# Performance work log

Hardware: AMD Instinct MI355X
Metric: run time of the kernel (lower is better)

Reference implementation:

```python
import jax, jax.numpy as jnp
import numpy as np

N = 50000      # nodes
E = 800000     # edges (before self-loops)
IN = 512       # in_dim
HID = 128      # hidden_dim
HEADS = 4
NEG_SLOPE = 0.2


def setup_inputs() -> dict:
    key = jax.random.key(0)
    ks = jax.random.split(key, 20)
    s = 0.05
    inp = {
        'x': jax.random.normal(ks[0], (N, IN), jnp.float32),
        'edge_index': jax.random.randint(ks[1], (2, E), 0, N, dtype=jnp.int32),
        # layer 0: GATConv(IN -> HID, heads=HEADS)
        'W0': jax.random.normal(ks[2], (HEADS * HID, IN), jnp.float32) * s,
        'a_src0': jax.random.normal(ks[3], (HEADS, HID), jnp.float32) * s,
        'a_dst0': jax.random.normal(ks[4], (HEADS, HID), jnp.float32) * s,
        'b0': jnp.zeros((HEADS * HID,), jnp.float32),
        # layer 1: GATConv(HEADS*HID -> HID, heads=HEADS)
        'W1': jax.random.normal(ks[5], (HEADS * HID, HEADS * HID), jnp.float32) * s,
        'a_src1': jax.random.normal(ks[6], (HEADS, HID), jnp.float32) * s,
        'a_dst1': jax.random.normal(ks[7], (HEADS, HID), jnp.float32) * s,
        'b1': jnp.zeros((HEADS * HID,), jnp.float32),
        # layer 2: GATConv(HEADS*HID -> HID, heads=1)
        'W2': jax.random.normal(ks[8], (HID, HEADS * HID), jnp.float32) * s,
        'a_src2': jax.random.normal(ks[9], (1, HID), jnp.float32) * s,
        'a_dst2': jax.random.normal(ks[10], (1, HID), jnp.float32) * s,
        'b2': jnp.zeros((HID,), jnp.float32),
        # output heads
        'Wv': jax.random.normal(ks[11], (HID, HID), jnp.float32) * s,
        'bv': jnp.zeros((HID,), jnp.float32),
        'Wt': jax.random.normal(ks[12], (HID, HID), jnp.float32) * s,
        'bt': jnp.zeros((HID,), jnp.float32),
    }
    return inp


def _gat_conv(x, src, dst, W, a_src, a_dst, bias, heads, n_nodes):
    """PyG-style GATConv (eval mode, att_dropout=0, self-loops pre-added)."""
    ch = a_src.shape[-1]
    h = (x @ W.T).reshape(n_nodes, heads, ch)            # [N,H,C]
    alpha_s = jnp.einsum('nhc,hc->nh', h, a_src)          # [N,H]
    alpha_d = jnp.einsum('nhc,hc->nh', h, a_dst)          # [N,H]
    e = alpha_s[src] + alpha_d[dst]                       # [E,H]
    e = jnp.where(e > 0, e, NEG_SLOPE * e)                # leaky_relu(0.2)
    # segment softmax over destination nodes
    m = jax.ops.segment_max(e, dst, num_segments=n_nodes)  # [N,H]
    e = jnp.exp(e - m[dst])
    z = jax.ops.segment_sum(e, dst, num_segments=n_nodes)  # [N,H]
    alpha = e / (z[dst] + 1e-16)                          # [E,H]
    msg = h[src] * alpha[:, :, None]                      # [E,H,C]
    out = jax.ops.segment_sum(msg, dst, num_segments=n_nodes)  # [N,H,C]
    return out.reshape(n_nodes, heads * ch) + bias


def reference(x, edge_index, W0, a_src0, a_dst0, b0, W1, a_src1, a_dst1, b1,
              W2, a_src2, a_dst2, b2, Wv, bv, Wt, bt):
    n = x.shape[0]
    loops = jnp.arange(n, dtype=edge_index.dtype)
    src = jnp.concatenate([edge_index[0], loops])
    dst = jnp.concatenate([edge_index[1], loops])

    h = _gat_conv(x, src, dst, W0, a_src0, a_dst0, b0, HEADS, n)
    h = jax.nn.relu(h)                                    # dropout is no-op in eval
    h = _gat_conv(h, src, dst, W1, a_src1, a_dst1, b1, HEADS, n)
    h = jax.nn.relu(h)
    h = _gat_conv(h, src, dst, W2, a_src2, a_dst2, b2, 1, n)  # [N,HID]

    x_vision = jax.nn.relu(h @ Wv.T + bv)
    x_text = jax.nn.relu(h @ Wt.T + bt)
    return (h, x_vision, x_text)
```

## Files before the change

### kernel.cpp

```cpp
#include <hip/hip_runtime.h>
#include <hip/hip_bf16.h>
#include <math.h>

typedef __bf16 bf16;
typedef __bf16 bf16x2 __attribute__((ext_vector_type(2)));
typedef __bf16 bf16x8 __attribute__((ext_vector_type(8)));
typedef float f32x4 __attribute__((ext_vector_type(4)));

#define NNODES 50000
#define NEDGES 800000

static __device__ __forceinline__ void gld_lds16(const void* g, void* l) {
    __builtin_amdgcn_global_load_lds((__attribute__((address_space(1))) void*)g,
                                     (__attribute__((address_space(3))) void*)l,
                                     16, 0, 0);
}

__global__ void detect_kernel(const unsigned int* __restrict__ xw, int* __restrict__ flag)
{
    const int l = threadIdx.x;
    int c = 0;
    for (int i = l; i < 4096; i += 64) {
        const unsigned int b1 = (xw[i] >> 8) & 0x7Fu;
        c += (b1 >= 0x34u && b1 <= 0x43u) ? 1 : 0;
    }
#pragma unroll
    for (int off = 32; off; off >>= 1) c += __shfl_xor(c, off);
    if (l == 0) *flag = (c < 2048) ? 1 : 0;
}

__global__ __launch_bounds__(256) void zero_out_kernel(void* out, long n, const int* __restrict__ flag)
{
    const int fp32 = *flag;
    const long i = (long)blockIdx.x * 256 + threadIdx.x;
    if (i < n) {
        if (fp32) ((float*)out)[i] = 0.f;
        else ((bf16*)out)[i] = (bf16)0.f;
    }
}

__global__ __launch_bounds__(256) void convert_kernel(
    const void* __restrict__ in, bf16* __restrict__ out, int n, const int* __restrict__ flag)
{
    const int fp32 = *flag;
    const int i = blockIdx.x * 256 + threadIdx.x;
    if (i >= n) return;
    out[i] = fp32 ? (bf16)(((const float*)in)[i]) : ((const bf16*)in)[i];
}

struct CvtBatch { const void* in[16]; bf16* out[16]; int n[16]; };

__global__ __launch_bounds__(256) void convert_batch_kernel(CvtBatch b, const int* __restrict__ flag)
{
    const int fp32 = *flag;
    const int it = blockIdx.y;
    const int n = b.n[it];
    const void* in = b.in[it];
    bf16* out = b.out[it];
    for (int i = blockIdx.x * 256 + threadIdx.x; i < n; i += gridDim.x * 256)
        out[i] = fp32 ? (bf16)(((const float*)in)[i]) : ((const bf16*)in)[i];
}

__global__ __launch_bounds__(256) void gemm_bt(
    const bf16* __restrict__ A, const bf16* __restrict__ B,
    bf16* __restrict__ C, int M, int N, int K)
{
    __shared__ __align__(16) bf16 As[128 * 32];
    __shared__ __align__(16) bf16 Bs[128 * 32];
    const int tid  = threadIdx.x;
    const int lane = tid & 63;
    const int w    = tid >> 6;
    const int wm   = (w >> 1) * 64, wn = (w & 1) * 64;
    const int mBase = blockIdx.y * 128, nBase = blockIdx.x * 128;

    f32x4 acc[4][4];
#pragma unroll
    for (int i = 0; i < 4; i++)
#pragma unroll
        for (int j = 0; j < 4; j++)
#pragma unroll
            for (int r = 0; r < 4; r++) acc[i][j][r] = 0.f;

    const int rA   = tid >> 2;
    const int kseg = (tid & 3) * 8;
    int ra0 = mBase + rA;       if (ra0 > M - 1) ra0 = M - 1;
    int ra1 = mBase + rA + 64;  if (ra1 > M - 1) ra1 = M - 1;
    const bf16* gA0 = A + (long)ra0 * K + kseg;
    const bf16* gA1 = A + (long)ra1 * K + kseg;
    const bf16* gB0 = B + (long)(nBase + rA) * K + kseg;
    const bf16* gB1 = B + (long)(nBase + rA + 64) * K + kseg;
    bf16* lA0 = &As[tid * 8];
    bf16* lA1 = &As[(tid + 256) * 8];
    bf16* lB0 = &Bs[tid * 8];
    bf16* lB1 = &Bs[(tid + 256) * 8];

    const int quad = lane >> 4, l16 = lane & 15;

    for (int k0 = 0; k0 < K; k0 += 32) {
        gld_lds16(gA0 + k0, lA0);
        gld_lds16(gA1 + k0, lA1);
        gld_lds16(gB0 + k0, lB0);
        gld_lds16(gB1 + k0, lB1);
        __syncthreads();
        bf16x8 af[4], bfr[4];
#pragma unroll
        for (int i = 0; i < 4; i++) {
            af[i]  = *(const bf16x8*)&As[(wm + i * 16 + l16) * 32 + quad * 8];
            bfr[i] = *(const bf16x8*)&Bs[(wn + i * 16 + l16) * 32 + quad * 8];
        }
#pragma unroll
        for (int i = 0; i < 4; i++)
#pragma unroll
            for (int j = 0; j < 4; j++)
                acc[i][j] = __builtin_amdgcn_mfma_f32_16x16x32_bf16(af[i], bfr[j], acc[i][j], 0, 0, 0);
        __syncthreads();
    }

#pragma unroll
    for (int i = 0; i < 4; i++) {
        const int row0 = mBase + wm + i * 16 + quad * 4;
#pragma unroll
        for (int j = 0; j < 4; j++) {
            const int colg = nBase + wn + j * 16 + l16;
#pragma unroll
            for (int r = 0; r < 4; r++) {
                const int row = row0 + r;
                if (row < M) C[(long)row * N + colg] = (bf16)acc[i][j][r];
            }
        }
    }
}

template <int H>
__global__ __launch_bounds__(H * 64) void alpha_kernel(
    const bf16* __restrict__ h, const bf16* __restrict__ av,
    const bf16* __restrict__ dv, float* __restrict__ as_out,
    float* __restrict__ ad_out)
{
    const int C = 128, HC = H * C;
    const int n = blockIdx.x;
    const int t = threadIdx.x;
    const int ht = t >> 6, l = t & 63;
    const bf16x2 hv = *(const bf16x2*)(h  + (long)n * HC + ht * C + 2 * l);
    const bf16x2 a2 = *(const bf16x2*)(av + ht * C + 2 * l);
    const bf16x2 d2 = *(const bf16x2*)(dv + ht * C + 2 * l);
    const float h0 = (float)hv[0], h1 = (float)hv[1];
    float ps = h0 * (float)a2[0] + h1 * (float)a2[1];
    float pd = h0 * (float)d2[0] + h1 * (float)d2[1];
#pragma unroll
    for (int off = 32; off; off >>= 1) {
        ps += __shfl_xor(ps, off);
        pd += __shfl_xor(pd, off);
    }
    if (l == 0) {
        as_out[(long)n * H + ht] = ps;
        ad_out[(long)n * H + ht] = pd;
    }
}

__global__ void hist_kernel(const int* __restrict__ dst, int* __restrict__ cnt, int E)
{
    const int e = blockIdx.x * blockDim.x + threadIdx.x;
    if (e < E) atomicAdd(&cnt[dst[e]], 1);
}

__global__ __launch_bounds__(256) void scan1_kernel(
    const int* __restrict__ cnt, int* __restrict__ rowptr, int* __restrict__ blksum, int n)
{
    __shared__ int buf[256];
    const int b = blockIdx.x, t = threadIdx.x, i = b * 256 + t;
    const int v = (i < n) ? cnt[i] : 0;
    buf[t] = v;
    __syncthreads();
    for (int off = 1; off < 256; off <<= 1) {
        const int add = (t >= off) ? buf[t - off] : 0;
        __syncthreads();
        buf[t] += add;
        __syncthreads();
    }
    if (i < n) rowptr[i + 1] = buf[t];
    if (t == 255) blksum[b] = buf[255];
    if (b == 0 && t == 0) rowptr[0] = 0;
}

__global__ __launch_bounds__(256) void scan2_kernel(int* __restrict__ blksum, int nb)
{
    __shared__ int buf[256];
    const int t = threadIdx.x;
    const int v = (t < nb) ? blksum[t] : 0;
    buf[t] = v;
    __syncthreads();
    for (int off = 1; off < 256; off <<= 1) {
        const int add = (t >= off) ? buf[t - off] : 0;
        __syncthreads();
        buf[t] += add;
        __syncthreads();
    }
    if (t < nb) blksum[t] = buf[t] - v;
}

__global__ __launch_bounds__(256) void scan3_kernel(
    int* __restrict__ rowptr, const int* __restrict__ blksum, int n)
{
    const int b = blockIdx.x, i = b * 256 + threadIdx.x;
    if (i < n) rowptr[i + 1] += blksum[b];
}

__global__ void fill_kernel(const int* __restrict__ src, const int* __restrict__ dst,
                            const int* __restrict__ rowptr, int* __restrict__ off,
                            int* __restrict__ col, int E)
{
    const int e = blockIdx.x * blockDim.x + threadIdx.x;
    if (e < E) {
        const int d = dst[e];
        const int p = rowptr[d] + atomicAdd(&off[d], 1);
        col[p] = src[e];
    }
}

__global__ __launch_bounds__(256) void agg4s_kernel(
    const bf16* __restrict__ h, const float* __restrict__ asrc,
    const float* __restrict__ adst, const int* __restrict__ rowptr,
    const int* __restrict__ col, const bf16* __restrict__ bias,
    bf16* __restrict__ out, int NB)
{
    __shared__ int2 ew_s[4][64];
    const int w = threadIdx.x >> 6, lane = threadIdx.x & 63;
    const int g = lane >> 4, li = lane & 15;
    const int s = blockIdx.x / NB;
    const int n = (blockIdx.x % NB) * 4 + w;
    const float ad = adst[(long)n * 4 + s];
    const int start = rowptr[n];
    const int deg   = rowptr[n + 1] - start;
    const int total = deg + 1;

    float z = 0.f;
    float acc[8];
#pragma unroll
    for (int c = 0; c < 8; c++) acc[c] = 0.f;
    const bf16* hp = h + (long)s * 128 + li * 8;
    const int2* ews = ew_s[w];

    for (int base = 0; base < total; base += 64) {
        const int i = base + lane;
        const bool valid = i < total;
        const int sv = (i < deg) ? col[start + i] : n;
        float e = asrc[(long)sv * 4 + s] + ad;
        e = (e > 0.f) ? e : 0.2f * e;
        e = fminf(fmaxf(e, -60.f), 60.f);
        const float wv = valid ? __expf(e) : 0.f;
        ew_s[w][lane] = make_int2(sv, __float_as_int(wv));
        __builtin_amdgcn_wave_barrier();
        const int cnt = min(64, total - base);
#pragma unroll 2
        for (int j = 0; j < cnt; j += 4) {
            const int2 v = ews[j + g];
            const float ww = __int_as_float(v.y);
            z += ww;
            const bf16x8 hv = *(const bf16x8*)(hp + (long)v.x * 512);
#pragma unroll
            for (int c = 0; c < 8; c++) acc[c] += ww * (float)hv[c];
        }
        __builtin_amdgcn_wave_barrier();
    }

#pragma unroll
    for (int c = 0; c < 8; c++) {
        acc[c] += __shfl_xor(acc[c], 16);
        acc[c] += __shfl_xor(acc[c], 32);
    }
    z += __shfl_xor(z, 16);
    z += __shfl_xor(z, 32);

    if (g == 0) {
        const float rz = 1.f / (z + 1e-16f);
        const bf16x8 b8 = *(const bf16x8*)(bias + s * 128 + li * 8);
        bf16x8 ov;
#pragma unroll
        for (int c = 0; c < 8; c++)
            ov[c] = (bf16)fmaxf(acc[c] * rz + (float)b8[c], 0.f);
        *(bf16x8*)(out + (long)n * 512 + s * 128 + li * 8) = ov;
    }
}

__global__ __launch_bounds__(256) void agg1g_kernel(
    const bf16* __restrict__ h, const float* __restrict__ asrc,
    const float* __restrict__ adst, const int* __restrict__ rowptr,
    const int* __restrict__ col, const bf16* __restrict__ bias,
    void* __restrict__ outv, const int* __restrict__ dflag)
{
    __shared__ int2 ew_s[4][64];
    const int w = threadIdx.x >> 6, lane = threadIdx.x & 63;
    const int g = lane >> 4, li = lane & 15;
    const int n = blockIdx.x * 4 + w;
    if (n >= NNODES) return;
    const int fp32out = *dflag;
    const float ad = adst[n];
    const int start = rowptr[n];
    const int deg   = rowptr[n + 1] - start;
    const int total = deg + 1;

    float z = 0.f;
    float acc[8];
#pragma unroll
    for (int c = 0; c < 8; c++) acc[c] = 0.f;
    const bf16* hp = h + li * 8;
    const int2* ews = ew_s[w];

    for (int base = 0; base < total; base += 64) {
        const int i = base + lane;
        const bool valid = i < total;
        const int sv = (i < deg) ? col[start + i] : n;
        float e = asrc[sv] + ad;
        e = (e > 0.f) ? e : 0.2f * e;
        e = fminf(fmaxf(e, -60.f), 60.f);
        const float wv = valid ? __expf(e) : 0.f;
        ew_s[w][lane] = make_int2(sv, __float_as_int(wv));
        __builtin_amdgcn_wave_barrier();
        const int cnt = min(64, total - base);
#pragma unroll 2
        for (int j = 0; j < cnt; j += 4) {
            const int2 v = ews[j + g];
            const float ww = __int_as_float(v.y);
            z += ww;
            const bf16x8 hv = *(const bf16x8*)(hp + (long)v.x * 128);
#pragma unroll
            for (int c = 0; c < 8; c++) acc[c] += ww * (float)hv[c];
        }
        __builtin_amdgcn_wave_barrier();
    }

#pragma unroll
    for (int c = 0; c < 8; c++) {
        acc[c] += __shfl_xor(acc[c], 16);
        acc[c] += __shfl_xor(acc[c], 32);
    }
    z += __shfl_xor(z, 16);
    z += __shfl_xor(z, 32);

    if (g == 0) {
        const float rz = 1.f / (z + 1e-16f);
        float o[8];
#pragma unroll
        for (int c = 0; c < 8; c++)
            o[c] = acc[c] * rz + (float)bias[li * 8 + c];
        if (fp32out) {
            float* op = (float*)outv + (long)n * 128 + li * 8;
            f32x4 o0, o1;
#pragma unroll
            for (int c = 0; c < 4; c++) { o0[c] = o[c]; o1[c] = o[c + 4]; }
            *(f32x4*)op = o0;
            *(f32x4*)(op + 4) = o1;
        } else {
            bf16x8 ov;
#pragma unroll
            for (int c = 0; c < 8; c++) ov[c] = (bf16)o[c];
            *(bf16x8*)((bf16*)outv + (long)n * 128 + li * 8) = ov;
        }
    }
}

__global__ __launch_bounds__(256) void heads_kernel(
    const void* __restrict__ hbase, void* __restrict__ outv,
    const bf16* __restrict__ Wv, const bf16* __restrict__ bv,
    const bf16* __restrict__ Wt, const bf16* __restrict__ bt,
    const int* __restrict__ dflag, int N)
{
    const int fp32 = *dflag;
    __shared__ float hbuf[32][128];
    const int n0 = blockIdx.x * 32, t = threadIdx.x;
    for (int i = t; i < 32 * 128; i += 256) {
        const int node = n0 + (i >> 7), c = i & 127;
        float v = 0.f;
        if (node < N)
            v = fp32 ? ((const float*)hbase)[(long)node * 128 + c]
                     : (float)((const bf16*)hbase)[(long)node * 128 + c];
        hbuf[i >> 7][c] = v;
    }
    __syncthreads();
    const int m = t & 127;
    const bool vis = t < 128;
    const bf16* W = vis ? Wv : Wt;
    const float b = (float)(vis ? bv[m] : bt[m]);
    float acc[32];
#pragma unroll
    for (int i = 0; i < 32; i++) acc[i] = 0.f;
    for (int k0 = 0; k0 < 128; k0 += 8) {
        const bf16x8 wv8 = *(const bf16x8*)&W[m * 128 + k0];
#pragma unroll
        for (int kk = 0; kk < 8; kk++) {
            const float wk = (float)wv8[kk];
#pragma unroll
            for (int i = 0; i < 32; i++) acc[i] += hbuf[i][k0 + kk] * wk;
        }
    }
    const long sec = vis ? (long)N * 128 : (long)2 * N * 128;
#pragma unroll
    for (int i = 0; i < 32; i++) {
        const int node = n0 + i;
        if (node < N) {
            float o = fmaxf(acc[i] + b, 0.f);
            const long idx = sec + (long)node * 128 + m;
            if (fp32) ((float*)outv)[idx] = o;
            else ((bf16*)outv)[idx] = (bf16)o;
        }
    }
}

extern "C" void kernel_launch(void* const* d_in, const int* in_sizes, int n_in,
                              void* d_out, int out_size, void* d_ws, size_t ws_size,
                              hipStream_t stream)
{
    const int N = NNODES, E = NEDGES;
    const int* srcp = (const int*)d_in[1];
    const int* dstp = srcp + E;

    char* p0 = (char*)d_ws;
    char* p = p0;
    auto bump = [&](size_t b) { char* r = p; p += (b + 255) & ~(size_t)255; return r; };
    int*   dflag  = (int*)bump(256);
    bf16*  xc     = (bf16*)bump((size_t)N * 512 * 2);
    bf16*  W0c    = (bf16*)bump(262144 * 2);
    bf16*  as0c   = (bf16*)bump(512 * 2);
    bf16*  ad0c   = (bf16*)bump(512 * 2);
    bf16*  b0c    = (bf16*)bump(512 * 2);
    bf16*  W1c    = (bf16*)bump(262144 * 2);
    bf16*  as1c   = (bf16*)bump(512 * 2);
    bf16*  ad1c   = (bf16*)bump(512 * 2);
    bf16*  b1c    = (bf16*)bump(512 * 2);
    bf16*  W2c    = (bf16*)bump(65536 * 2);
    bf16*  as2c   = (bf16*)bump(128 * 2);
    bf16*  ad2c   = (bf16*)bump(128 * 2);
    bf16*  b2c    = (bf16*)bump(128 * 2);
    bf16*  Wvc    = (bf16*)bump(16384 * 2);
    bf16*  bvc    = (bf16*)bump(128 * 2);
    bf16*  Wtc    = (bf16*)bump(16384 * 2);
    bf16*  btc    = (bf16*)bump(128 * 2);
    int*   cnt    = (int*)bump((size_t)N * 4);
    int*   offs   = (int*)bump((size_t)N * 4);
    int*   rowptr = (int*)bump((size_t)(N + 1) * 4);
    int*   blksum = (int*)bump(256 * 4);
    int*   colarr = (int*)bump((size_t)E * 4);
    float* alphaS = (float*)bump((size_t)N * 4 * 4);
    float* alphaD = (float*)bump((size_t)N * 4 * 4);
    bf16*  bufA   = (bf16*)bump((size_t)N * 512 * 2);
    bf16*  bufB   = (bf16*)bump((size_t)N * 512 * 2);
    const size_t need = (size_t)(p - p0);

    detect_kernel<<<1, 64, 0, stream>>>((const unsigned int*)d_in[0], dflag);

    if (need > ws_size) {
        zero_out_kernel<<<((long)out_size + 255) / 256, 256, 0, stream>>>(d_out, out_size, dflag);
        return;
    }

    convert_kernel<<<(N * 512 + 255) / 256, 256, 0, stream>>>(d_in[0], xc, N * 512, dflag);
    CvtBatch cb;
    const void* ins[16] = {d_in[2], d_in[3], d_in[4], d_in[5], d_in[6], d_in[7], d_in[8], d_in[9],
                           d_in[10], d_in[11], d_in[12], d_in[13], d_in[14], d_in[15], d_in[16], d_in[17]};
    bf16* outs[16] = {W0c, as0c, ad0c, b0c, W1c, as1c, ad1c, b1c,
                      W2c, as2c, ad2c, b2c, Wvc, bvc, Wtc, btc};
    const int ns[16] = {262144, 512, 512, 512, 262144, 512, 512, 512,
                        65536, 128, 128, 128, 16384, 128, 16384, 128};
    for (int i = 0; i < 16; i++) { cb.in[i] = ins[i]; cb.out[i] = outs[i]; cb.n[i] = ns[i]; }
    convert_batch_kernel<<<dim3(256, 16), 256, 0, stream>>>(cb, dflag);

    const int nb = (N + 255) / 256;
    hipMemsetAsync(cnt, 0, (size_t)N * 4, stream);
    hipMemsetAsync(offs, 0, (size_t)N * 4, stream);
    hist_kernel<<<(E + 255) / 256, 256, 0, stream>>>(dstp, cnt, E);
    scan1_kernel<<<nb, 256, 0, stream>>>(cnt, rowptr, blksum, N);
    scan2_kernel<<<1, 256, 0, stream>>>(blksum, nb);
    scan3_kernel<<<nb, 256, 0, stream>>>(rowptr, blksum, N);
    fill_kernel<<<(E + 255) / 256, 256, 0, stream>>>(srcp, dstp, rowptr, offs, colarr, E);

    const int NB = N / 4;

    dim3 g0(4, (N + 127) / 128);
    gemm_bt<<<g0, 256, 0, stream>>>(xc, W0c, bufA, N, 512, 512);
    alpha_kernel<4><<<N, 256, 0, stream>>>(bufA, as0c, ad0c, alphaS, alphaD);
    agg4s_kernel<<<NB * 4, 256, 0, stream>>>(bufA, alphaS, alphaD, rowptr, colarr, b0c, bufB, NB);

    gemm_bt<<<g0, 256, 0, stream>>>(bufB, W1c, bufA, N, 512, 512);
    alpha_kernel<4><<<N, 256, 0, stream>>>(bufA, as1c, ad1c, alphaS, alphaD);
    agg4s_kernel<<<NB * 4, 256, 0, stream>>>(bufA, alphaS, alphaD, rowptr, colarr, b1c, bufB, NB);

    dim3 g2(1, (N + 127) / 128);
    gemm_bt<<<g2, 256, 0, stream>>>(bufB, W2c, bufA, N, 128, 512);
    alpha_kernel<1><<<N, 64, 0, stream>>>(bufA, as2c, ad2c, alphaS, alphaD);
    agg1g_kernel<<<(N + 3) / 4, 256, 0, stream>>>(bufA, alphaS, alphaD, rowptr, colarr, b2c, d_out, dflag);

    heads_kernel<<<(N + 31) / 32, 256, 0, stream>>>(d_out, d_out, Wvc, bvc, Wtc, btc, dflag, N);
}
```

Measured before the change: 863.1 us.

## Fuse attention-score dot products into GEMM epilogue, vectorize converts, unroll gathers

The per-node alpha kernels are removed, and the attention source/destination dot products are now computed in the GEMM epilogue from the accumulators, reduced by shuffles and LDS atomics. This avoids re-reading the projected features and saves three launches. The input conversion kernels now process four elements per thread. The aggregation loops prescale neighbor indices into byte offsets and issue four independent gathers per iteration to raise memory-level parallelism. The epilogue adds register pressure and a shared-memory atomic step to the GEMM.

```diff
diff --git a/kernel.cpp b/kernel.cpp
--- a/kernel.cpp
+++ b/kernel.cpp
@@ -4,6 +4,7 @@
 
 typedef __bf16 bf16;
 typedef __bf16 bf16x2 __attribute__((ext_vector_type(2)));
+typedef __bf16 bf16x4 __attribute__((ext_vector_type(4)));
 typedef __bf16 bf16x8 __attribute__((ext_vector_type(8)));
 typedef float f32x4 __attribute__((ext_vector_type(4)));
 
@@ -39,39 +40,59 @@
     }
 }
 
-__global__ __launch_bounds__(256) void convert_kernel(
-    const void* __restrict__ in, bf16* __restrict__ out, int n, const int* __restrict__ flag)
+__global__ __launch_bounds__(256) void convert4_kernel(
+    const void* __restrict__ in, bf16* __restrict__ out, int n4, const int* __restrict__ flag)
 {
     const int fp32 = *flag;
     const int i = blockIdx.x * 256 + threadIdx.x;
-    if (i >= n) return;
-    out[i] = fp32 ? (bf16)(((const float*)in)[i]) : ((const bf16*)in)[i];
-}
-
-struct CvtBatch { const void* in[16]; bf16* out[16]; int n[16]; };
+    if (i >= n4) return;
+    bf16x4 o;
+    if (fp32) {
+        const float4 v = ((const float4*)in)[i];
+        o[0] = (bf16)v.x; o[1] = (bf16)v.y; o[2] = (bf16)v.z; o[3] = (bf16)v.w;
+    } else {
+        o = ((const bf16x4*)in)[i];
+    }
+    ((bf16x4*)out)[i] = o;
+}
+
+struct CvtBatch { const void* in[16]; bf16* out[16]; int n4[16]; };
 
 __global__ __launch_bounds__(256) void convert_batch_kernel(CvtBatch b, const int* __restrict__ flag)
 {
     const int fp32 = *flag;
     const int it = blockIdx.y;
-    const int n = b.n[it];
+    const int n4 = b.n4[it];
     const void* in = b.in[it];
     bf16* out = b.out[it];
-    for (int i = blockIdx.x * 256 + threadIdx.x; i < n; i += gridDim.x * 256)
-        out[i] = fp32 ? (bf16)(((const float*)in)[i]) : ((const bf16*)in)[i];
+    for (int i = blockIdx.x * 256 + threadIdx.x; i < n4; i += gridDim.x * 256) {
+        bf16x4 o;
+        if (fp32) {
+            const float4 v = ((const float4*)in)[i];
+            o[0] = (bf16)v.x; o[1] = (bf16)v.y; o[2] = (bf16)v.z; o[3] = (bf16)v.w;
+        } else {
+            o = ((const bf16x4*)in)[i];
+        }
+        ((bf16x4*)out)[i] = o;
+    }
 }
 
 __global__ __launch_bounds__(256) void gemm_bt(
     const bf16* __restrict__ A, const bf16* __restrict__ B,
-    bf16* __restrict__ C, int M, int N, int K)
+    bf16* __restrict__ C, int M, int N, int K,
+    const bf16* __restrict__ av, const bf16* __restrict__ dv,
+    float* __restrict__ aS, float* __restrict__ aD, int H)
 {
     __shared__ __align__(16) bf16 As[128 * 32];
     __shared__ __align__(16) bf16 Bs[128 * 32];
+    __shared__ float sPS[128];
+    __shared__ float sPD[128];
     const int tid  = threadIdx.x;
     const int lane = tid & 63;
     const int w    = tid >> 6;
     const int wm   = (w >> 1) * 64, wn = (w & 1) * 64;
     const int mBase = blockIdx.y * 128, nBase = blockIdx.x * 128;
+    const int hb = nBase >> 7;
 
     f32x4 acc[4][4];
 #pragma unroll
@@ -96,6 +117,8 @@
 
     const int quad = lane >> 4, l16 = lane & 15;
 
+    if (tid < 128) { sPS[tid] = 0.f; sPD[tid] = 0.f; }
+
     for (int k0 = 0; k0 < K; k0 += 32) {
         gld_lds16(gA0 + k0, lA0);
         gld_lds16(gA1 + k0, lA1);
@@ -116,6 +139,36 @@
         __syncthreads();
     }
 
+    float aval[4], dval[4];
+#pragma unroll
+    for (int j = 0; j < 4; j++) {
+        const int cg = nBase + wn + j * 16 + l16;
+        aval[j] = (float)av[cg];
+        dval[j] = (float)dv[cg];
+    }
+#pragma unroll
+    for (int i = 0; i < 4; i++) {
+#pragma unroll
+        for (int r = 0; r < 4; r++) {
+            float ps = 0.f, pd = 0.f;
+#pragma unroll
+            for (int j = 0; j < 4; j++) {
+                ps += acc[i][j][r] * aval[j];
+                pd += acc[i][j][r] * dval[j];
+            }
+#pragma unroll
+            for (int off = 8; off; off >>= 1) {
+                ps += __shfl_xor(ps, off);
+                pd += __shfl_xor(pd, off);
+            }
+            if (l16 == 0) {
+                const int rl = wm + i * 16 + quad * 4 + r;
+                atomicAdd(&sPS[rl], ps);
+                atomicAdd(&sPD[rl], pd);
+            }
+        }
+    }
+
 #pragma unroll
     for (int i = 0; i < 4; i++) {
         const int row0 = mBase + wm + i * 16 + quad * 4;
@@ -129,32 +182,14 @@
             }
         }
     }
-}
-
-template <int H>
-__global__ __launch_bounds__(H * 64) void alpha_kernel(
-    const bf16* __restrict__ h, const bf16* __restrict__ av,
-    const bf16* __restrict__ dv, float* __restrict__ as_out,
-    float* __restrict__ ad_out)
-{
-    const int C = 128, HC = H * C;
-    const int n = blockIdx.x;
-    const int t = threadIdx.x;
-    const int ht = t >> 6, l = t & 63;
-    const bf16x2 hv = *(const bf16x2*)(h  + (long)n * HC + ht * C + 2 * l);
-    const bf16x2 a2 = *(const bf16x2*)(av + ht * C + 2 * l);
-    const bf16x2 d2 = *(const bf16x2*)(dv + ht * C + 2 * l);
-    const float h0 = (float)hv[0], h1 = (float)hv[1];
-    float ps = h0 * (float)a2[0] + h1 * (float)a2[1];
-    float pd = h0 * (float)d2[0] + h1 * (float)d2[1];
-#pragma unroll
-    for (int off = 32; off; off >>= 1) {
-        ps += __shfl_xor(ps, off);
-        pd += __shfl_xor(pd, off);
-    }
-    if (l == 0) {
-        as_out[(long)n * H + ht] = ps;
-        ad_out[(long)n * H + ht] = pd;
+
+    __syncthreads();
+    if (tid < 128) {
+        const int row = mBase + tid;
+        if (row < M) {
+            aS[(long)row * H + hb] = sPS[tid];
+            aD[(long)row * H + hb] = sPD[tid];
+        }
     }
 }
 
@@ -238,7 +273,8 @@
     float acc[8];
 #pragma unroll
     for (int c = 0; c < 8; c++) acc[c] = 0.f;
-    const bf16* hp = h + (long)s * 128 + li * 8;
+    const char* hbp = (const char*)h;
+    const int sOff = s * 256 + li * 16;
     const int2* ews = ew_s[w];
 
     for (int base = 0; base < total; base += 64) {
@@ -249,15 +285,35 @@
         e = (e > 0.f) ? e : 0.2f * e;
         e = fminf(fmaxf(e, -60.f), 60.f);
         const float wv = valid ? __expf(e) : 0.f;
-        ew_s[w][lane] = make_int2(sv, __float_as_int(wv));
+        ew_s[w][lane] = make_int2(sv << 10, __float_as_int(wv));
         __builtin_amdgcn_wave_barrier();
         const int cnt = min(64, total - base);
-#pragma unroll 2
-        for (int j = 0; j < cnt; j += 4) {
+        int j = 0;
+        for (; j + 16 <= cnt; j += 16) {
+            const int2 v0 = ews[j + g];
+            const int2 v1 = ews[j + 4 + g];
+            const int2 v2 = ews[j + 8 + g];
+            const int2 v3 = ews[j + 12 + g];
+            const bf16x8 h0 = *(const bf16x8*)(hbp + (v0.x + sOff));
+            const bf16x8 h1 = *(const bf16x8*)(hbp + (v1.x + sOff));
+            const bf16x8 h2 = *(const bf16x8*)(hbp + (v2.x + sOff));
+            const bf16x8 h3 = *(const bf16x8*)(hbp + (v3.x + sOff));
+            const float w0 = __int_as_float(v0.y), w1 = __int_as_float(v1.y);
+            const float w2 = __int_as_float(v2.y), w3 = __int_as_float(v3.y);
+            z += w0 + w1 + w2 + w3;
+#pragma unroll
+            for (int c = 0; c < 8; c++) {
+                acc[c] += w0 * (float)h0[c];
+                acc[c] += w1 * (float)h1[c];
+                acc[c] += w2 * (float)h2[c];
+                acc[c] += w3 * (float)h3[c];
+            }
+        }
+        for (; j < cnt; j += 4) {
             const int2 v = ews[j + g];
             const float ww = __int_as_float(v.y);
             z += ww;
-            const bf16x8 hv = *(const bf16x8*)(hp + (long)v.x * 512);
+            const bf16x8 hv = *(const bf16x8*)(hbp + (v.x + sOff));
 #pragma unroll
             for (int c = 0; c < 8; c++) acc[c] += ww * (float)hv[c];
         }
@@ -304,7 +360,8 @@
     float acc[8];
 #pragma unroll
     for (int c = 0; c < 8; c++) acc[c] = 0.f;
-    const bf16* hp = h + li * 8;
+    const char* hbp = (const char*)h;
+    const int sOff = li * 16;
     const int2* ews = ew_s[w];
 
     for (int base = 0; base < total; base += 64) {
@@ -315,15 +372,35 @@
         e = (e > 0.f) ? e : 0.2f * e;
         e = fminf(fmaxf(e, -60.f), 60.f);
         const float wv = valid ? __expf(e) : 0.f;
-        ew_s[w][lane] = make_int2(sv, __float_as_int(wv));
+        ew_s[w][lane] = make_int2(sv << 8, __float_as_int(wv));
         __builtin_amdgcn_wave_barrier();
         const int cnt = min(64, total - base);
-#pragma unroll 2
-        for (int j = 0; j < cnt; j += 4) {
+        int j = 0;
+        for (; j + 16 <= cnt; j += 16) {
+            const int2 v0 = ews[j + g];
+            const int2 v1 = ews[j + 4 + g];
+            const int2 v2 = ews[j + 8 + g];
+            const int2 v3 = ews[j + 12 + g];
+            const bf16x8 h0 = *(const bf16x8*)(hbp + (v0.x + sOff));
+            const bf16x8 h1 = *(const bf16x8*)(hbp + (v1.x + sOff));
+            const bf16x8 h2 = *(const bf16x8*)(hbp + (v2.x + sOff));
+            const bf16x8 h3 = *(const bf16x8*)(hbp + (v3.x + sOff));
+            const float w0 = __int_as_float(v0.y), w1 = __int_as_float(v1.y);
+            const float w2 = __int_as_float(v2.y), w3 = __int_as_float(v3.y);
+            z += w0 + w1 + w2 + w3;
+#pragma unroll
+            for (int c = 0; c < 8; c++) {
+                acc[c] += w0 * (float)h0[c];
+                acc[c] += w1 * (float)h1[c];
+                acc[c] += w2 * (float)h2[c];
+                acc[c] += w3 * (float)h3[c];
+            }
+        }
+        for (; j < cnt; j += 4) {
             const int2 v = ews[j + g];
             const float ww = __int_as_float(v.y);
             z += ww;
-            const bf16x8 hv = *(const bf16x8*)(hp + (long)v.x * 128);
+            const bf16x8 hv = *(const bf16x8*)(hbp + (v.x + sOff));
 #pragma unroll
             for (int c = 0; c < 8; c++) acc[c] += ww * (float)hv[c];
         }
@@ -454,16 +531,16 @@
         return;
     }
 
-    convert_kernel<<<(N * 512 + 255) / 256, 256, 0, stream>>>(d_in[0], xc, N * 512, dflag);
+    convert4_kernel<<<(N * 512 / 4 + 255) / 256, 256, 0, stream>>>(d_in[0], xc, N * 512 / 4, dflag);
     CvtBatch cb;
     const void* ins[16] = {d_in[2], d_in[3], d_in[4], d_in[5], d_in[6], d_in[7], d_in[8], d_in[9],
                            d_in[10], d_in[11], d_in[12], d_in[13], d_in[14], d_in[15], d_in[16], d_in[17]};
     bf16* outs[16] = {W0c, as0c, ad0c, b0c, W1c, as1c, ad1c, b1c,
                       W2c, as2c, ad2c, b2c, Wvc, bvc, Wtc, btc};
-    const int ns[16] = {262144, 512, 512, 512, 262144, 512, 512, 512,
-                        65536, 128, 128, 128, 16384, 128, 16384, 128};
-    for (int i = 0; i < 16; i++) { cb.in[i] = ins[i]; cb.out[i] = outs[i]; cb.n[i] = ns[i]; }
-    convert_batch_kernel<<<dim3(256, 16), 256, 0, stream>>>(cb, dflag);
+    const int ns4[16] = {65536, 128, 128, 128, 65536, 128, 128, 128,
+                         16384, 32, 32, 32, 4096, 32, 4096, 32};
+    for (int i = 0; i < 16; i++) { cb.in[i] = ins[i]; cb.out[i] = outs[i]; cb.n4[i] = ns4[i]; }
+    convert_batch_kernel<<<dim3(64, 16), 256, 0, stream>>>(cb, dflag);
 
     const int nb = (N + 255) / 256;
     hipMemsetAsync(cnt, 0, (size_t)N * 4, stream);
@@ -477,17 +554,17 @@
     const int NB = N / 4;
 
     dim3 g0(4, (N + 127) / 128);
-    gemm_bt<<<g0, 256, 0, stream>>>(xc, W0c, bufA, N, 512, 512);
-    alpha_kernel<4><<<N, 256, 0, stream>>>(bufA, as0c, ad0c, alphaS, alphaD);
+    gemm_bt<<<g0, 256, 0, stream>>>(xc, W0c, bufA, N, 512, 512,
+                                    as0c, ad0c, alphaS, alphaD, 4);
     agg4s_kernel<<<NB * 4, 256, 0, stream>>>(bufA, alphaS, alphaD, rowptr, colarr, b0c, bufB, NB);
 
-    gemm_bt<<<g0, 256, 0, stream>>>(bufB, W1c, bufA, N, 512, 512);
-    alpha_kernel<4><<<N, 256, 0, stream>>>(bufA, as1c, ad1c, alphaS, alphaD);
+    gemm_bt<<<g0, 256, 0, stream>>>(bufB, W1c, bufA, N, 512, 512,
+                                    as1c, ad1c, alphaS, alphaD, 4);
     agg4s_kernel<<<NB * 4, 256, 0, stream>>>(bufA, alphaS, alphaD, rowptr, colarr, b1c, bufB, NB);
 
     dim3 g2(1, (N + 127) / 128);
-    gemm_bt<<<g2, 256, 0, stream>>>(bufB, W2c, bufA, N, 128, 512);
-    alpha_kernel<1><<<N, 64, 0, stream>>>(bufA, as2c, ad2c, alphaS, alphaD);
+    gemm_bt<<<g2, 256, 0, stream>>>(bufB, W2c, bufA, N, 128, 512,
+                                    as2c, ad2c, alphaS, alphaD, 1);
     agg1g_kernel<<<(N + 3) / 4, 256, 0, stream>>>(bufA, alphaS, alphaD, rowptr, colarr, b2c, d_out, dflag);
 
     heads_kernel<<<(N + 31) / 32, 256, 0, stream>>>(d_out, d_out, Wvc, bvc, Wtc, btc, dflag, N);
```

After: 817.0 us. 1.06x faster.
